# Performance work log

Hardware: AMD Instinct MI355X
Metric: run time of the kernel (lower is better)

The kernel has to match this reference:

```python
import jax, jax.numpy as jnp
import numpy as np

T = 2048
HID = 2048
H = 16
NOPE = 128
ROPE = 64
QKD = NOPE + ROPE  # 192
VD = 128
QLR = 1536
KVLR = 512
IDX_H = 32
IDX_D = 128
TOPK = 512
EPS = 1e-6
SCALING = QKD ** -0.5


def rms_norm(x, w):
    return x * jax.lax.rsqrt(jnp.mean(x * x, axis=-1, keepdims=True) + EPS) * w


def layer_norm(x, g, b):
    mu = jnp.mean(x, axis=-1, keepdims=True)
    var = jnp.mean((x - mu) ** 2, axis=-1, keepdims=True)
    return (x - mu) * jax.lax.rsqrt(var + EPS) * g + b


def apply_rope(x, positions, base=10000.0):
    # non-neox (interleaved) rotary; x: [..., d] with leading token axis
    d = x.shape[-1]
    inv = 1.0 / (base ** (jnp.arange(0, d, 2, dtype=jnp.float32) / d))
    f = positions.astype(jnp.float32)[:, None] * inv  # [T, d/2]
    shp = (x.shape[0],) + (1,) * (x.ndim - 2) + (d // 2,)
    cos, sin = jnp.cos(f).reshape(shp), jnp.sin(f).reshape(shp)
    x1, x2 = x[..., ::2], x[..., 1::2]
    return jnp.stack([x1 * cos - x2 * sin, x1 * sin + x2 * cos], axis=-1).reshape(x.shape)


def setup_inputs() -> dict:
    key = jax.random.key(0)
    ks = jax.random.split(key, 10)
    s = 0.02
    return {
        "positions": jnp.arange(T, dtype=jnp.int64) if jax.config.jax_enable_x64 else jnp.arange(T, dtype=jnp.int32),
        "hidden_states": jax.random.normal(ks[0], (T, HID), jnp.float32),
        "w_qkv_a": jax.random.normal(ks[1], (HID, QLR + KVLR + ROPE), jnp.float32) * s,
        "q_a_ln_w": jnp.ones((QLR,), jnp.float32),
        "w_qb": jax.random.normal(ks[2], (QLR, H * QKD), jnp.float32) * s,
        "kv_a_ln_w": jnp.ones((KVLR,), jnp.float32),
        "w_kvb": jax.random.normal(ks[3], (KVLR, H * (NOPE + VD)), jnp.float32) * s,
        "w_o": jax.random.normal(ks[4], (H * VD, HID), jnp.float32) * s,
        "w_idx_qb": jax.random.normal(ks[5], (QLR, IDX_H * IDX_D), jnp.float32) * s,
        "w_idx_k": jax.random.normal(ks[6], (HID, IDX_D), jnp.float32) * s,
        "idx_k_gamma": jnp.ones((IDX_D,), jnp.float32),
        "idx_k_beta": jnp.zeros((IDX_D,), jnp.float32),
        "w_wproj": jax.random.normal(ks[7], (HID, IDX_H), jnp.float32) * s,
        "b_wproj": jnp.zeros((IDX_H,), jnp.float32),
    }


def _forward(positions, hidden_states, w_qkv_a, q_a_ln_w, w_qb, kv_a_ln_w, w_kvb,
             w_o, w_idx_qb, w_idx_k, idx_k_gamma, idx_k_beta, w_wproj, b_wproj):
    t = hidden_states.shape[0]
    # fused low-rank projections
    qkv = hidden_states @ w_qkv_a
    q_c, kv_c, k_pe = jnp.split(qkv, [QLR, QLR + KVLR], axis=-1)
    q_c = rms_norm(q_c, q_a_ln_w)           # hidden_states_or_q_c
    kv_cn = rms_norm(kv_c, kv_a_ln_w)

    # ---- Indexer (lightning top-k token selection) ----
    qi = (q_c @ w_idx_qb).reshape(t, IDX_H, IDX_D)
    qi_pe, qi_nope = qi[..., :ROPE], qi[..., ROPE:]
    ki = layer_norm(hidden_states @ w_idx_k, idx_k_gamma, idx_k_beta)  # [T, IDX_D]
    ki_pe, ki_nope = ki[..., :ROPE], ki[..., ROPE:]
    qi = jnp.concatenate([apply_rope(qi_pe, positions), qi_nope], axis=-1)
    ki = jnp.concatenate([apply_rope(ki_pe, positions), ki_nope], axis=-1)
    w = (hidden_states @ w_wproj + b_wproj) * (IDX_D ** -0.5) * (IDX_H ** -0.5)  # [T, IDX_H]
    logits = jax.nn.relu(jnp.einsum('thd,sd->ths', qi, ki))   # [T, IDX_H, T]
    score = jnp.einsum('th,ths->ts', w, logits)               # [T, T]
    causal = jnp.tril(jnp.ones((t, t), bool))
    neg = jnp.finfo(score.dtype).min
    score = jnp.where(causal, score, neg)
    _, topk_idx = jax.lax.top_k(score, TOPK)                  # [T, TOPK]
    sel = jnp.zeros((t, t), bool).at[jnp.arange(t)[:, None], topk_idx].set(True)
    mask = causal & sel

    # ---- MLA attention ----
    q = (q_c @ w_qb).reshape(t, H, QKD)
    q_nope, q_pe = q[..., :NOPE], q[..., NOPE:]
    q_pe = apply_rope(q_pe, positions)
    k_pe_r = apply_rope(k_pe, positions)                      # [T, ROPE], shared across heads
    kv = (kv_cn @ w_kvb).reshape(t, H, NOPE + VD)
    k_nope, v = kv[..., :NOPE], kv[..., NOPE:]
    q_full = jnp.concatenate([q_nope, q_pe], axis=-1)         # [T, H, QKD]
    k_full = jnp.concatenate([k_nope, jnp.broadcast_to(k_pe_r[:, None, :], (t, H, ROPE))], axis=-1)
    attn = jnp.einsum('thd,shd->hts', q_full, k_full) * SCALING
    attn = jnp.where(mask[None], attn, neg)
    p = jax.nn.softmax(attn, axis=-1)
    out = jnp.einsum('hts,shv->thv', p, v).reshape(t, H * VD)
    return out @ w_o


def reference(positions, hidden_states, w_qkv_a, q_a_ln_w, w_qb, kv_a_ln_w, w_kvb,
              w_o, w_idx_qb, w_idx_k, idx_k_gamma, idx_k_beta, w_wproj, b_wproj):
    return _forward(positions, hidden_states, w_qkv_a, q_a_ln_w, w_qb, kv_a_ln_w,
                    w_kvb, w_o, w_idx_qb, w_idx_k, idx_k_gamma, idx_k_beta,
                    w_wproj, b_wproj)
```

## Files before the change

### kernel.cpp

```cpp
#include <hip/hip_runtime.h>
#include <cfloat>
#include <cmath>

#define T_    2048
#define HID_  2048
#define QKVN_ 2112
#define QKVX_ 2272
#define QLR_  1536
#define KVLR_ 512
#define ROPE_ 64
#define NOPE_ 128
#define QKD_  192
#define VD_   128
#define H_    16
#define IDXH_ 32
#define IDXD_ 128
#define TOPK_ 512
#define EPS_  1e-6f
#define SCALING_ 0.07216878364870323f

typedef unsigned int u32;
typedef unsigned short u16;
typedef __bf16 bf16x8 __attribute__((ext_vector_type(8)));
typedef _Float16 f16;
typedef f16 f16x8 __attribute__((ext_vector_type(8)));
typedef float f32x4 __attribute__((ext_vector_type(4)));

__device__ __forceinline__ u16 f2bf(float x) {
  u32 u = __float_as_uint(x);
  u32 r = (u + 0x7fffu + ((u >> 16) & 1u)) >> 16;
  return (u16)r;
}
__device__ __forceinline__ float bf2f(u16 h) { return __uint_as_float(((u32)h) << 16); }
__device__ __forceinline__ u32 pack2(float a, float b) { return (u32)f2bf(a) | ((u32)f2bf(b) << 16); }
__device__ __forceinline__ bf16x8 ld8(const void* p) { return *(const bf16x8*)p; }
__device__ __forceinline__ f32x4 mfma16(bf16x8 a, bf16x8 b, f32x4 c) {
  return __builtin_amdgcn_mfma_f32_16x16x32_bf16(a, b, c, 0, 0, 0);
}
__device__ __forceinline__ u16 hbits(f16 h) { union { f16 h; u16 u; } c; c.h = h; return c.u; }
__device__ __forceinline__ u32 hpack(f16 a, f16 b) { return (u32)hbits(a) | ((u32)hbits(b) << 16); }
__device__ __forceinline__ f16x8 ldh8(const void* p) { return *(const f16x8*)p; }
__device__ __forceinline__ f32x4 mfmah(f16x8 a, f16x8 b, f32x4 c) {
  return __builtin_amdgcn_mfma_f32_16x16x32_f16(a, b, c, 0, 0, 0);
}
__device__ __forceinline__ void gload16(const u16* g, u16* l) {
  __builtin_amdgcn_global_load_lds(
      (__attribute__((address_space(1))) void*)(g),
      (__attribute__((address_space(3))) void*)(l), 16, 0, 0);
}

__global__ __launch_bounds__(256) void rope_tab_kernel(float2* __restrict__ tab) {
  int i = blockIdx.x * 256 + threadIdx.x;
  if (i >= T_ * 32) return;
  int t = i >> 5, j = i & 31;
  float inv = powf(10000.f, -(float)j * (1.f / 32.f));
  float f = (float)t * inv;
  tab[i] = make_float2(cosf(f), sinf(f));
}
__device__ __forceinline__ void rope_apply(float2 cs, float& x0, float& x1) {
  float a = x0, b = x1;
  x0 = a * cs.x - b * cs.y;
  x1 = a * cs.y + b * cs.x;
}

struct TSJob { const float* src; u16* oh; u16* ol; int K; int N; };
__global__ __launch_bounds__(256) void transpose_split_multi(
    TSJob j0, TSJob j1, TSJob j2, TSJob j3) {
  TSJob jb = (blockIdx.z == 0) ? j0 : (blockIdx.z == 1) ? j1 : (blockIdx.z == 2) ? j2 : j3;
  int k0 = blockIdx.y * 64, n0 = blockIdx.x * 64;
  if (k0 >= jb.K || n0 >= jb.N) return;
  __shared__ float t[64][65];
  for (int j = 0; j < 16; ++j) {
    int u = threadIdx.x + 256 * j; int r = u >> 6, c = u & 63;
    t[r][c] = (k0 + r < jb.K && n0 + c < jb.N) ? jb.src[(size_t)(k0 + r) * jb.N + n0 + c] : 0.f;
  }
  __syncthreads();
  for (int j = 0; j < 16; ++j) {
    int u = threadIdx.x + 256 * j; int r = u >> 6, c = u & 63;
    if (n0 + r < jb.N && k0 + c < jb.K) {
      float v = t[c][r];
      f16 h = (f16)v;
      jb.oh[(size_t)(n0 + r) * jb.K + k0 + c] = hbits(h);
      jb.ol[(size_t)(n0 + r) * jb.K + k0 + c] = hbits((f16)(v - (float)h));
    }
  }
}

struct TBJob { const float* src; u16* out; int K; int N; };
__global__ __launch_bounds__(256) void transpose_bf16_multi(TBJob j0, TBJob j1, TBJob j2) {
  TBJob jb = (blockIdx.z == 0) ? j0 : (blockIdx.z == 1) ? j1 : j2;
  int k0 = blockIdx.y * 64, n0 = blockIdx.x * 64;
  if (k0 >= jb.K || n0 >= jb.N) return;
  __shared__ float t[64][65];
  for (int j = 0; j < 16; ++j) {
    int u = threadIdx.x + 256 * j; int r = u >> 6, c = u & 63;
    t[r][c] = (k0 + r < jb.K && n0 + c < jb.N) ? jb.src[(size_t)(k0 + r) * jb.N + n0 + c] : 0.f;
  }
  __syncthreads();
  for (int j = 0; j < 16; ++j) {
    int u = threadIdx.x + 256 * j; int r = u >> 6, c = u & 63;
    if (n0 + r < jb.N && k0 + c < jb.K) jb.out[(size_t)(n0 + r) * jb.K + k0 + c] = f2bf(t[c][r]);
  }
}

__global__ __launch_bounds__(256) void split_f16_k(
    const float* __restrict__ in, u16* __restrict__ hi, u16* __restrict__ lo, long n) {
  for (long i = ((long)blockIdx.x * 256 + threadIdx.x) * 4; i < n; i += (long)gridDim.x * 1024) {
    float4 v = *(const float4*)(in + i);
    f16 a = (f16)v.x, b = (f16)v.y, c = (f16)v.z, d = (f16)v.w;
    *(u32*)(hi + i) = hpack(a, b);
    *(u32*)(hi + i + 2) = hpack(c, d);
    *(u32*)(lo + i) = hpack((f16)(v.x - (float)a), (f16)(v.y - (float)b));
    *(u32*)(lo + i + 2) = hpack((f16)(v.z - (float)c), (f16)(v.w - (float)d));
  }
}

__global__ __launch_bounds__(256) void conv_bf16_k(
    const float* __restrict__ in, u16* __restrict__ out, long n) {
  for (long i = ((long)blockIdx.x * 256 + threadIdx.x) * 4; i < n; i += (long)gridDim.x * 1024) {
    float4 v = *(const float4*)(in + i);
    *(u32*)(out + i) = pack2(v.x, v.y);
    *(u32*)(out + i + 2) = pack2(v.z, v.w);
  }
}

__global__ __launch_bounds__(256) void gemm_hl(
    const u16* __restrict__ Ah_, const u16* __restrict__ Al_, int lda,
    const u16* __restrict__ Bh_, const u16* __restrict__ Bl_, int ldb,
    float* __restrict__ C, int ldc, const float* __restrict__ bias, int bcol0,
    float bscale, int N, int K) {
  __shared__ u32 Ah[128][16], Al[128][16], Bh[128][16], Bl[128][16];
  const int tid = threadIdx.x;
  const int bm = blockIdx.y * 128, bn = blockIdx.x * 128;
  const int wid = tid >> 6, lane = tid & 63, wr = wid >> 1, wc = wid & 1;
  const int lr = lane & 15, lg = lane >> 4;
  const u16* srcb = (wid == 0) ? Ah_ : (wid == 1) ? Al_ : (wid == 2) ? Bh_ : Bl_;
  const int sld = (wid < 2) ? lda : ldb;
  const int rb = (wid < 2) ? bm : bn;
  u16* dst = (u16*)((wid == 0) ? &Ah[0][0] : (wid == 1) ? &Al[0][0]
                                           : (wid == 2) ? &Bh[0][0] : &Bl[0][0]);
  const int rowl = lane >> 2;
  const int offl = (lane & 3) * 8;
  f32x4 acc[4][4] = {};
  for (int k0 = 0; k0 < K; k0 += 32) {
#pragma unroll
    for (int c = 0; c < 8; ++c) {
      int gr = rb + c * 16 + rowl;
      if (wid >= 2) gr = min(gr, N - 1);
      gload16(srcb + (size_t)gr * sld + k0 + offl, dst + c * 512);
    }
    __syncthreads();
    f16x8 ah[4], al[4], bh[4], bl[4];
#pragma unroll
    for (int i = 0; i < 4; ++i) {
      ah[i] = ldh8(&Ah[wr * 64 + i * 16 + lr][lg * 4]);
      al[i] = ldh8(&Al[wr * 64 + i * 16 + lr][lg * 4]);
      bh[i] = ldh8(&Bh[wc * 64 + i * 16 + lr][lg * 4]);
      bl[i] = ldh8(&Bl[wc * 64 + i * 16 + lr][lg * 4]);
    }
#pragma unroll
    for (int i = 0; i < 4; ++i)
#pragma unroll
      for (int jn = 0; jn < 4; ++jn) {
        acc[i][jn] = mfmah(ah[i], bh[jn], acc[i][jn]);
        acc[i][jn] = mfmah(ah[i], bl[jn], acc[i][jn]);
        acc[i][jn] = mfmah(al[i], bh[jn], acc[i][jn]);
      }
    __syncthreads();
  }
#pragma unroll
  for (int i = 0; i < 4; ++i)
#pragma unroll
    for (int jn = 0; jn < 4; ++jn)
#pragma unroll
      for (int j = 0; j < 4; ++j) {
        int row = bm + wr * 64 + i * 16 + lg * 4 + j;
        int col = bn + wc * 64 + jn * 16 + lr;
        if (col < N) {
          float v = acc[i][jn][j];
          if (col >= bcol0) v = (v + bias[col - bcol0]) * bscale;
          C[(size_t)row * ldc + col] = v;
        }
      }
}

template <int CBF16>
__global__ __launch_bounds__(256) void gemm_t(
    const u16* __restrict__ Ab, int lda, long aoz,
    const u16* __restrict__ Bt, int ldb, long boz,
    void* __restrict__ Cp, int ldc, long coz, int N, int K) {
  __shared__ u32 As[128][16], Bs[128][16];
  const int tid = threadIdx.x;
  const int z = blockIdx.z;
  const int bm = blockIdx.y * 128, bn = blockIdx.x * 128;
  const int wid = tid >> 6, lane = tid & 63, wr = wid >> 1, wc = wid & 1;
  const int lr = lane & 15, lg = lane >> 4;
  const u16* A = Ab + aoz * z;
  const u16* B = Bt + boz * z;
  const u16* srcb = (wid < 2) ? A : B;
  const int sld = (wid < 2) ? lda : ldb;
  const int rb = (wid < 2) ? bm : bn;
  u16* dst = (u16*)((wid < 2) ? &As[0][0] : &Bs[0][0]);
  const int ccb = (wid & 1) * 4;
  const int rowl = lane >> 2;
  const int offl = (lane & 3) * 8;
  f32x4 acc[4][4] = {};
  for (int k0 = 0; k0 < K; k0 += 32) {
#pragma unroll
    for (int c = 0; c < 4; ++c) {
      int cc = ccb + c;
      int gr = rb + cc * 16 + rowl;
      if (wid >= 2) gr = min(gr, N - 1);
      gload16(srcb + (size_t)gr * sld + k0 + offl, dst + cc * 512);
    }
    __syncthreads();
    bf16x8 af[4], bf[4];
#pragma unroll
    for (int i = 0; i < 4; ++i) {
      af[i] = ld8(&As[wr * 64 + i * 16 + lr][lg * 4]);
      bf[i] = ld8(&Bs[wc * 64 + i * 16 + lr][lg * 4]);
    }
#pragma unroll
    for (int i = 0; i < 4; ++i)
#pragma unroll
      for (int jn = 0; jn < 4; ++jn)
        acc[i][jn] = mfma16(af[i], bf[jn], acc[i][jn]);
    __syncthreads();
  }
#pragma unroll
  for (int i = 0; i < 4; ++i)
#pragma unroll
    for (int jn = 0; jn < 4; ++jn)
#pragma unroll
      for (int j = 0; j < 4; ++j) {
        int row = bm + wr * 64 + i * 16 + lg * 4 + j;
        int col = bn + wc * 64 + jn * 16 + lr;
        if (col < N) {
          if (CBF16) ((u16*)Cp)[coz * z + (size_t)row * ldc + col] = f2bf(acc[i][jn][j]);
          else ((float*)Cp)[coz * z + (size_t)row * ldc + col] = acc[i][jn][j];
        }
      }
}

__global__ __launch_bounds__(256) void rmsnorm_kernel(
    const float* __restrict__ qkvx, const float* __restrict__ qw,
    const float* __restrict__ kvw, u16* __restrict__ qcb,
    u16* __restrict__ qch, u16* __restrict__ qcl, u16* __restrict__ kv_cn) {
  const int t = blockIdx.x, tid = threadIdx.x;
  const float* row = qkvx + (size_t)t * QKVX_;
  __shared__ float red[256];
  float ss = 0.f;
  for (int i = tid; i < QLR_; i += 256) { float v = row[i]; ss += v * v; }
  red[tid] = ss; __syncthreads();
  for (int s = 128; s; s >>= 1) { if (tid < s) red[tid] += red[tid + s]; __syncthreads(); }
  float scl = 1.0f / sqrtf(red[0] / (float)QLR_ + EPS_);
  for (int i = tid; i < QLR_; i += 256) {
    float val = row[i] * scl * qw[i];
    qcb[(size_t)t * QLR_ + i] = f2bf(val);
    f16 h = (f16)val;
    qch[(size_t)t * QLR_ + i] = hbits(h);
    qcl[(size_t)t * QLR_ + i] = hbits((f16)(val - (float)h));
  }
  __syncthreads();
  ss = 0.f;
  for (int i = tid; i < KVLR_; i += 256) { float v = row[QLR_ + i]; ss += v * v; }
  red[tid] = ss; __syncthreads();
  for (int s = 128; s; s >>= 1) { if (tid < s) red[tid] += red[tid + s]; __syncthreads(); }
  scl = 1.0f / sqrtf(red[0] / (float)KVLR_ + EPS_);
  for (int i = tid; i < KVLR_; i += 256)
    kv_cn[(size_t)t * KVLR_ + i] = f2bf(row[QLR_ + i] * scl * kvw[i]);
}

__global__ __launch_bounds__(256) void rope_qi_split_kernel(
    const float* __restrict__ qi, const float2* __restrict__ tab,
    u16* __restrict__ qih, u16* __restrict__ qil) {
  const int t = blockIdx.x, tid = threadIdx.x;
  const float* src = qi + (size_t)t * (IDXH_ * IDXD_);
  u16* dh = qih + (size_t)t * (IDXH_ * IDXD_);
  u16* dl = qil + (size_t)t * (IDXH_ * IDXD_);
  for (int p = tid; p < IDXH_ * IDXD_ / 2; p += 256) {
    int d = p & 63;
    float x0 = src[2 * p], x1 = src[2 * p + 1];
    if (d < 32) rope_apply(tab[t * 32 + d], x0, x1);
    f16 h0 = (f16)x0, h1 = (f16)x1;
    *(u32*)(dh + 2 * p) = hpack(h0, h1);
    *(u32*)(dl + 2 * p) = hpack((f16)(x0 - (float)h0), (f16)(x1 - (float)h1));
  }
}

__global__ __launch_bounds__(256) void rope_q_bf_kernel(
    u16* __restrict__ qfb, const float2* __restrict__ tab) {
  const int t = blockIdx.x, tid = threadIdx.x;
  for (int idx = tid; idx < H_ * 32; idx += 256) {
    int hh = idx / 32, j = idx % 32;
    u16* p = qfb + (size_t)t * (H_ * QKD_) + hh * QKD_ + NOPE_ + 2 * j;
    float x0 = bf2f(p[0]), x1 = bf2f(p[1]);
    rope_apply(tab[t * 32 + j], x0, x1);
    p[0] = f2bf(x0); p[1] = f2bf(x1);
  }
}

__global__ __launch_bounds__(64) void rope_kpe_kernel(
    const float* __restrict__ qkvx, const float2* __restrict__ tab,
    u16* __restrict__ kper) {
  const int t = blockIdx.x, tid = threadIdx.x;
  if (tid >= 32) return;
  const float* p = qkvx + (size_t)t * QKVX_ + (QLR_ + KVLR_);
  float x0 = p[2 * tid], x1 = p[2 * tid + 1];
  rope_apply(tab[t * 32 + tid], x0, x1);
  kper[(size_t)t * ROPE_ + 2 * tid] = f2bf(x0);
  kper[(size_t)t * ROPE_ + 2 * tid + 1] = f2bf(x1);
}

__global__ __launch_bounds__(128) void ki_ln_rope_kernel(
    const float* __restrict__ qkvx, const float* __restrict__ gamma,
    const float* __restrict__ beta, const float2* __restrict__ tab,
    u16* __restrict__ kih, u16* __restrict__ kil) {
  const int t = blockIdx.x, tid = threadIdx.x;
  __shared__ float x[128];
  __shared__ float red[128];
  float v = qkvx[(size_t)t * QKVX_ + QKVN_ + tid];
  red[tid] = v; __syncthreads();
  for (int s = 64; s; s >>= 1) { if (tid < s) red[tid] += red[tid + s]; __syncthreads(); }
  float mu = red[0] / 128.f;
  __syncthreads();
  float d = v - mu;
  red[tid] = d * d; __syncthreads();
  for (int s = 64; s; s >>= 1) { if (tid < s) red[tid] += red[tid + s]; __syncthreads(); }
  float var = red[0] / 128.f;
  float y = d * (1.0f / sqrtf(var + EPS_)) * gamma[tid] + beta[tid];
  x[tid] = y; __syncthreads();
  if (tid < 32) {
    float x0 = x[2 * tid], x1 = x[2 * tid + 1];
    rope_apply(tab[t * 32 + tid], x0, x1);
    x[2 * tid] = x0; x[2 * tid + 1] = x1;
  }
  __syncthreads();
  float fv = x[tid];
  f16 h = (f16)fv;
  kih[(size_t)t * IDXD_ + tid] = hbits(h);
  kil[(size_t)t * IDXD_ + tid] = hbits((f16)(fv - (float)h));
}

__global__ __launch_bounds__(256) void score_mfma(
    const u16* __restrict__ qih, const u16* __restrict__ qil,
    const u16* __restrict__ kih, const u16* __restrict__ kil,
    const float* __restrict__ wgt, int ldw, float* __restrict__ score) {
  const int s0 = blockIdx.x * 64, t0 = blockIdx.y * 64;
  if (s0 > t0 + 63) return;
  __shared__ u32 Kh[64][68], Kl[64][68], Qh[64][68], Ql[64][68];
  __shared__ float wts[64][33];
  const int tid = threadIdx.x;
  const int wid = tid >> 6, lane = tid & 63, wr = wid >> 1, wc = wid & 1;
  const int lr = lane & 15, lg = lane >> 4;
#pragma unroll
  for (int j = 0; j < 4; ++j) {
    int u = tid + 256 * j; int row = u >> 4, p = u & 15;
    *(uint4*)&Kh[row][p * 4] = *(const uint4*)(kih + (size_t)(s0 + row) * IDXD_ + p * 8);
    *(uint4*)&Kl[row][p * 4] = *(const uint4*)(kil + (size_t)(s0 + row) * IDXD_ + p * 8);
  }
#pragma unroll
  for (int j = 0; j < 8; ++j) {
    int u = tid + 256 * j; int r = u >> 5, c = u & 31;
    wts[r][c] = wgt[(size_t)(t0 + r) * ldw + c];
  }
  __syncthreads();
  f16x8 bh[2][4], bl[2][4];
#pragma unroll
  for (int ni = 0; ni < 2; ++ni)
#pragma unroll
    for (int kb = 0; kb < 4; ++kb) {
      bh[ni][kb] = ldh8(&Kh[wc * 32 + ni * 16 + lr][kb * 16 + lg * 4]);
      bl[ni][kb] = ldh8(&Kl[wc * 32 + ni * 16 + lr][kb * 16 + lg * 4]);
    }
  f32x4 fin[2][2] = {};
  for (int h = 0; h < IDXH_; ++h) {
#pragma unroll
    for (int j = 0; j < 4; ++j) {
      int u = tid + 256 * j; int row = u >> 4, p = u & 15;
      size_t g = (size_t)(t0 + row) * (IDXH_ * IDXD_) + h * IDXD_ + p * 8;
      *(uint4*)&Qh[row][p * 4] = *(const uint4*)(qih + g);
      *(uint4*)&Ql[row][p * 4] = *(const uint4*)(qil + g);
    }
    __syncthreads();
    f32x4 acch[2][2] = {};
#pragma unroll
    for (int kb = 0; kb < 4; ++kb) {
      f16x8 ah0 = ldh8(&Qh[wr * 32 + lr][kb * 16 + lg * 4]);
      f16x8 ah1 = ldh8(&Qh[wr * 32 + 16 + lr][kb * 16 + lg * 4]);
      f16x8 al0 = ldh8(&Ql[wr * 32 + lr][kb * 16 + lg * 4]);
      f16x8 al1 = ldh8(&Ql[wr * 32 + 16 + lr][kb * 16 + lg * 4]);
#pragma unroll
      for (int ni = 0; ni < 2; ++ni) {
        acch[0][ni] = mfmah(ah0, bh[ni][kb], acch[0][ni]);
        acch[0][ni] = mfmah(ah0, bl[ni][kb], acch[0][ni]);
        acch[0][ni] = mfmah(al0, bh[ni][kb], acch[0][ni]);
        acch[1][ni] = mfmah(ah1, bh[ni][kb], acch[1][ni]);
        acch[1][ni] = mfmah(ah1, bl[ni][kb], acch[1][ni]);
        acch[1][ni] = mfmah(al1, bh[ni][kb], acch[1][ni]);
      }
    }
#pragma unroll
    for (int mi = 0; mi < 2; ++mi)
#pragma unroll
      for (int j = 0; j < 4; ++j) {
        float w = wts[wr * 32 + mi * 16 + lg * 4 + j][h];
        fin[mi][0][j] += w * fmaxf(acch[mi][0][j], 0.f);
        fin[mi][1][j] += w * fmaxf(acch[mi][1][j], 0.f);
      }
    __syncthreads();
  }
#pragma unroll
  for (int mi = 0; mi < 2; ++mi)
#pragma unroll
    for (int ni = 0; ni < 2; ++ni)
#pragma unroll
      for (int j = 0; j < 4; ++j) {
        int row = t0 + wr * 32 + mi * 16 + lg * 4 + j;
        int col = s0 + wc * 32 + ni * 16 + lr;
        score[(size_t)row * T_ + col] = fin[mi][ni][j];
      }
}

__global__ __launch_bounds__(256) void topk_kernel(
    const float* __restrict__ score, int* __restrict__ selidx,
    int* __restrict__ selcnt) {
  const int t = blockIdx.x;
  const int L = t + 1;
  const int tid = threadIdx.x;
  if (L <= TOPK_) {
    for (int j = tid; j < TOPK_; j += 256)
      selidx[(size_t)t * TOPK_ + j] = (j < L) ? j : 0;
    if (tid == 0) selcnt[t] = L;
    return;
  }
  __shared__ unsigned u[T_];
  __shared__ unsigned hist[16];
  __shared__ unsigned sprefix;
  __shared__ int sk;
  __shared__ int part[256];
  for (int i = tid; i < T_; i += 256) {
    float v = (i < L) ? score[(size_t)t * T_ + i] : -FLT_MAX;
    unsigned b = __float_as_uint(v);
    u[i] = (b & 0x80000000u) ? ~b : (b | 0x80000000u);
  }
  if (tid == 0) { sprefix = 0u; sk = TOPK_; }
  __syncthreads();
  for (int pass = 0; pass < 8; ++pass) {
    const int shift = 28 - 4 * pass;
    if (tid < 16) hist[tid] = 0u;
    __syncthreads();
    unsigned pfx = sprefix;
    for (int i = tid; i < L; i += 256) {
      unsigned val = u[i];
      bool match = (pass == 0) || ((val >> (shift + 4)) == pfx);
      if (match) atomicAdd(&hist[(val >> shift) & 15u], 1u);
    }
    __syncthreads();
    if (tid == 0) {
      int k = sk; unsigned cum = 0u; int bsel = 0;
      for (int bb = 15; bb >= 0; --bb) {
        if (cum + hist[bb] >= (unsigned)k) { bsel = bb; sk = k - (int)cum; break; }
        cum += hist[bb];
      }
      sprefix = (sprefix << 4) | (unsigned)bsel;
    }
    __syncthreads();
  }
  const unsigned thr = sprefix;
  const int kEq = sk;
  const int base = tid * 8;
  int eqloc[8]; int esum = 0;
  for (int r = 0; r < 8; ++r) {
    int i = base + r;
    int f = (i < L && u[i] == thr) ? 1 : 0;
    eqloc[r] = esum; esum += f;
  }
  part[tid] = esum; __syncthreads();
  for (int off = 1; off < 256; off <<= 1) {
    int v = (tid >= off) ? part[tid - off] : 0;
    __syncthreads();
    part[tid] += v;
    __syncthreads();
  }
  const int ebase = (tid > 0) ? part[tid - 1] : 0;
  __syncthreads();
  int sloc[8], selflag[8]; int ssum = 0;
  for (int r = 0; r < 8; ++r) {
    int i = base + r;
    int f = 0;
    if (i < L) {
      unsigned ui = u[i];
      if (ui > thr) f = 1;
      else if (ui == thr && (ebase + eqloc[r]) < kEq) f = 1;
    }
    selflag[r] = f; sloc[r] = ssum; ssum += f;
  }
  part[tid] = ssum; __syncthreads();
  for (int off = 1; off < 256; off <<= 1) {
    int v = (tid >= off) ? part[tid - off] : 0;
    __syncthreads();
    part[tid] += v;
    __syncthreads();
  }
  const int sbase = (tid > 0) ? part[tid - 1] : 0;
  for (int r = 0; r < 8; ++r)
    if (selflag[r]) selidx[(size_t)t * TOPK_ + sbase + sloc[r]] = base + r;
  if (tid == 0) selcnt[t] = TOPK_;
}

__global__ __launch_bounds__(256, 3) void attn_mla_kernel(
    const u16* __restrict__ qeff, const u16* __restrict__ qfb,
    const u16* __restrict__ kvcn, const u16* __restrict__ kper,
    const int* __restrict__ selidx, const int* __restrict__ selcnt,
    u16* __restrict__ Olat) {
  const int t = blockIdx.x;
  const int tid = threadIdx.x;
  const int wid = tid >> 6, lane = tid & 63;
  const int lr = lane & 15, lg = lane >> 4;
  __shared__ int sidxs[512];
  __shared__ u16 Pb[16][520];
  __shared__ u16 SB[4][4096];
  __shared__ float redm[4][16];
  __shared__ float reds[4][16];
  const int cnt = selcnt[t];
  for (int j = tid; j < 512; j += 256) sidxs[j] = selidx[(size_t)t * TOPK_ + j];
  __syncthreads();

  const int kl = lane >> 2;
  const int pcs = (((lane & 3) ^ ((lane >> 3) & 3))) << 3;
  const int rsw = ((lr >> 1) & 3) << 3;
  int skey[8];
#pragma unroll
  for (int j = 0; j < 8; ++j) skey[j] = sidxs[wid * 128 + j * 16 + kl];
  u16* ksw = &SB[wid][0];

  const u16* qe = qeff + (size_t)t * (H_ * 512) + lr * 512 + lg * 8;
  const u16* qp = qfb + (size_t)t * (H_ * QKD_) + lr * QKD_ + NOPE_ + lg * 8;
  bf16x8 qf[18];
#pragma unroll
  for (int kb = 0; kb < 16; ++kb) qf[kb] = ld8(qe + kb * 32);
  qf[16] = ld8(qp);
  qf[17] = ld8(qp + 32);

  f32x4 lgv[8] = {};
#pragma unroll
  for (int kb = 0; kb < 18; ++kb) {
    if (kb < 16) {
#pragma unroll
      for (int j = 0; j < 8; ++j)
        gload16(kvcn + (size_t)skey[j] * 512 + kb * 32 + pcs, ksw + j * 512);
    } else {
#pragma unroll
      for (int j = 0; j < 8; ++j)
        gload16(kper + (size_t)skey[j] * 64 + (kb - 16) * 32 + pcs, ksw + j * 512);
    }
    asm volatile("s_waitcnt vmcnt(0)" ::: "memory");
    __builtin_amdgcn_sched_barrier(0);
#pragma unroll
    for (int m = 0; m < 8; ++m) {
      bf16x8 kf = ld8(ksw + (m * 16 + lr) * 32 + (lg * 8 ^ rsw));
      lgv[m] = mfma16(kf, qf[kb], lgv[m]);
    }
    asm volatile("s_waitcnt lgkmcnt(0)" ::: "memory");
    __builtin_amdgcn_sched_barrier(0);
  }

  float mx = -FLT_MAX;
#pragma unroll
  for (int m = 0; m < 8; ++m)
#pragma unroll
    for (int j = 0; j < 4; ++j) {
      int slot = wid * 128 + m * 16 + lg * 4 + j;
      float v = (slot < cnt) ? lgv[m][j] * SCALING_ : -FLT_MAX;
      lgv[m][j] = v;
      mx = fmaxf(mx, v);
    }
  mx = fmaxf(mx, __shfl_xor(mx, 16));
  mx = fmaxf(mx, __shfl_xor(mx, 32));
  if (lane < 16) redm[wid][lane] = mx;
  __syncthreads();
  float hm = fmaxf(fmaxf(redm[0][lr], redm[1][lr]), fmaxf(redm[2][lr], redm[3][lr]));
  float sm = 0.f;
#pragma unroll
  for (int m = 0; m < 8; ++m)
#pragma unroll
    for (int j = 0; j < 4; ++j) {
      int slot = wid * 128 + m * 16 + lg * 4 + j;
      float e = (slot < cnt) ? expf(lgv[m][j] - hm) : 0.f;
      lgv[m][j] = e; sm += e;
    }
  sm += __shfl_xor(sm, 16);
  sm += __shfl_xor(sm, 32);
  if (lane < 16) reds[wid][lane] = sm;
  __syncthreads();
  float inv = 1.f / (reds[0][lr] + reds[1][lr] + reds[2][lr] + reds[3][lr]);
#pragma unroll
  for (int m = 0; m < 8; ++m) {
    int sl = wid * 128 + m * 16 + lg * 4;
    *(u32*)&Pb[lr][sl] = pack2(lgv[m][0] * inv, lgv[m][1] * inv);
    *(u32*)&Pb[lr][sl + 2] = pack2(lgv[m][2] * inv, lgv[m][3] * inv);
  }
  __syncthreads();

  u32* vpw = (u32*)&SB[wid][0];
  const int pl = lane >> 4;
  const int gq = lane & 15;
  const u16* vsrc = kvcn + wid * 128 + gq * 8;
  f32x4 oacc[8] = {};
  uint4 ra[4], rb[4];
#pragma unroll
  for (int s = 0; s < 4; ++s) {
    int p = s * 4 + pl;
    ra[s] = *(const uint4*)(vsrc + (size_t)sidxs[2 * p] * 512);
    rb[s] = *(const uint4*)(vsrc + (size_t)sidxs[2 * p + 1] * 512);
  }
  for (int c = 0; c < 16; ++c) {
#pragma unroll
    for (int s = 0; s < 4; ++s) {
      int p = s * 4 + pl;
      int col = (gq * 8) ^ ((s & 3) << 3);
      const u16* A = (const u16*)&ra[s];
      const u16* B = (const u16*)&rb[s];
      u32 w[8];
#pragma unroll
      for (int j = 0; j < 8; ++j) w[j] = (u32)A[j] | ((u32)B[j] << 16);
      *(uint4*)&vpw[p * 128 + col] = make_uint4(w[0], w[1], w[2], w[3]);
      *(uint4*)&vpw[p * 128 + col + 4] = make_uint4(w[4], w[5], w[6], w[7]);
    }
    if (c < 15) {
#pragma unroll
      for (int s = 0; s < 4; ++s) {
        int p = s * 4 + pl;
        ra[s] = *(const uint4*)(vsrc + (size_t)sidxs[(c + 1) * 32 + 2 * p] * 512);
        rb[s] = *(const uint4*)(vsrc + (size_t)sidxs[(c + 1) * 32 + 2 * p + 1] * 512);
      }
    }
    bf16x8 pa = ld8(&Pb[lr][c * 32 + lg * 8]);
    union BB { u32 u[4]; bf16x8 v; };
    BB bb[8];
#pragma unroll
    for (int C = 0; C < 8; ++C) {
      int col = (C * 16 + lr) ^ (lg << 3);
#pragma unroll
      for (int e = 0; e < 4; ++e)
        bb[C].u[e] = vpw[(lg * 4 + e) * 128 + col];
    }
    __builtin_amdgcn_s_setprio(1);
#pragma unroll
    for (int C = 0; C < 8; ++C) oacc[C] = mfma16(pa, bb[C].v, oacc[C]);
    __builtin_amdgcn_s_setprio(0);
  }
#pragma unroll
  for (int C = 0; C < 8; ++C)
#pragma unroll
    for (int j = 0; j < 4; ++j) {
      int h = lg * 4 + j;
      Olat[(size_t)t * (H_ * 512) + h * 512 + wid * 128 + C * 16 + lr] = f2bf(oacc[C][j]);
    }
}

extern "C" void kernel_launch(void* const* d_in, const int* in_sizes, int n_in,
                              void* d_out, int out_size, void* d_ws, size_t ws_size,
                              hipStream_t stream) {
  const float* hidden    = (const float*)d_in[1];
  const float* w_qkv_a   = (const float*)d_in[2];
  const float* q_a_ln_w  = (const float*)d_in[3];
  const float* w_qb      = (const float*)d_in[4];
  const float* kv_a_ln_w = (const float*)d_in[5];
  const float* w_kvb     = (const float*)d_in[6];
  const float* w_o       = (const float*)d_in[7];
  const float* w_idx_qb  = (const float*)d_in[8];
  const float* w_idx_k   = (const float*)d_in[9];
  const float* idx_g     = (const float*)d_in[10];
  const float* idx_b     = (const float*)d_in[11];
  const float* w_wproj   = (const float*)d_in[12];
  const float* b_wproj   = (const float*)d_in[13];

  char* W = (char*)d_ws;
  size_t o = 0;
  auto alloc = [&](size_t bytes) { void* p = W + o; o += (bytes + 255) & ~(size_t)255; return p; };
  u16* qcb     = (u16*)alloc((size_t)T_ * QLR_ * 2);
  u16* kv_cn   = (u16*)alloc((size_t)T_ * KVLR_ * 2);
  u16* kper    = (u16*)alloc((size_t)T_ * ROPE_ * 2);
  int* selidx  = (int*)alloc((size_t)T_ * TOPK_ * 4);
  int* selcnt  = (int*)alloc((size_t)T_ * 4);
  u16* kih     = (u16*)alloc((size_t)T_ * IDXD_ * 2);
  u16* kil     = (u16*)alloc((size_t)T_ * IDXD_ * 2);
  u16* hidh    = (u16*)alloc((size_t)T_ * HID_ * 2);
  u16* hidl    = (u16*)alloc((size_t)T_ * HID_ * 2);
  float2* rtab = (float2*)alloc((size_t)T_ * 32 * 8);
  u16* qch     = (u16*)alloc((size_t)T_ * QLR_ * 2);
  u16* qcl     = (u16*)alloc((size_t)T_ * QLR_ * 2);
  u16* wiqh    = (u16*)alloc((size_t)(IDXH_ * IDXD_) * QLR_ * 2);
  u16* wiql    = (u16*)alloc((size_t)(IDXH_ * IDXD_) * QLR_ * 2);
  u16* qih     = qch;
  u16* qil     = qch + (size_t)T_ * IDXH_ * IDXD_;
  float* qi    = (float*)alloc((size_t)T_ * IDXH_ * IDXD_ * 4);
  u16* qeff    = (u16*)qi;
  float* score = (float*)alloc((size_t)T_ * T_ * 4);
  u16* qfb     = (u16*)score;
  u16* attno   = (u16*)score;
  u16* wcath   = (u16*)alloc((size_t)QKVX_ * HID_ * 2);
  u16* wcatl   = (u16*)alloc((size_t)QKVX_ * HID_ * 2);
  float* qkvx  = (float*)alloc((size_t)T_ * QKVX_ * 4);
  u16* Olat    = wcath;
  u16* wqbt    = (u16*)alloc((size_t)(H_ * QKD_) * QLR_ * 2);
  u16* wkvb    = (u16*)alloc((size_t)KVLR_ * (H_ * 256) * 2);
  u16* wkvbt   = (u16*)alloc((size_t)(H_ * 256) * KVLR_ * 2);
  u16* wot     = (u16*)alloc((size_t)(H_ * VD_) * HID_ * 2);

  dim3 blk(256);
  auto g2 = [](int M, int N, int Z) { return dim3((N + 127) / 128, M / 128, Z); };

  rope_tab_kernel<<<(T_ * 32 + 255) / 256, blk, 0, stream>>>(rtab);
  {
    TSJob j0{w_qkv_a, wcath, wcatl, HID_, QKVN_};
    TSJob j1{w_idx_qb, wiqh, wiql, QLR_, IDXH_ * IDXD_};
    TSJob j2{w_idx_k, wcath + (size_t)QKVN_ * HID_, wcatl + (size_t)QKVN_ * HID_, HID_, IDXD_};
    TSJob j3{w_wproj, wcath + (size_t)(QKVN_ + IDXD_) * HID_, wcatl + (size_t)(QKVN_ + IDXD_) * HID_, HID_, IDXH_};
    transpose_split_multi<<<dim3(64, 32, 4), blk, 0, stream>>>(j0, j1, j2, j3);
  }
  {
    TBJob j0{w_qb, wqbt, QLR_, H_ * QKD_};
    TBJob j1{w_kvb, wkvbt, KVLR_, H_ * 256};
    TBJob j2{w_o, wot, H_ * VD_, HID_};
    transpose_bf16_multi<<<dim3(64, 32, 3), blk, 0, stream>>>(j0, j1, j2);
  }
  split_f16_k<<<2048, blk, 0, stream>>>(hidden, hidh, hidl, (long)T_ * HID_);
  conv_bf16_k<<<2048, blk, 0, stream>>>(w_kvb, wkvb, (long)KVLR_ * H_ * 256);

  gemm_hl<<<g2(T_, QKVX_, 1), blk, 0, stream>>>(
      hidh, hidl, HID_, wcath, wcatl, HID_, qkvx, QKVX_,
      b_wproj, QKVN_ + IDXD_, 0.015625f, QKVX_, HID_);
  rmsnorm_kernel<<<T_, blk, 0, stream>>>(qkvx, q_a_ln_w, kv_a_ln_w, qcb, qch, qcl, kv_cn);
  rope_kpe_kernel<<<T_, 64, 0, stream>>>(qkvx, rtab, kper);
  ki_ln_rope_kernel<<<T_, 128, 0, stream>>>(qkvx, idx_g, idx_b, rtab, kih, kil);

  gemm_hl<<<g2(T_, IDXH_ * IDXD_, 1), blk, 0, stream>>>(
      qch, qcl, QLR_, wiqh, wiql, QLR_, qi, IDXH_ * IDXD_,
      nullptr, 1 << 30, 1.f, IDXH_ * IDXD_, QLR_);
  rope_qi_split_kernel<<<T_, blk, 0, stream>>>(qi, rtab, qih, qil);

  score_mfma<<<dim3(32, 32), blk, 0, stream>>>(qih, qil, kih, kil,
                                               qkvx + QKVN_ + IDXD_, QKVX_, score);
  topk_kernel<<<T_, blk, 0, stream>>>(score, selidx, selcnt);

  gemm_t<1><<<g2(T_, H_ * QKD_, 1), blk, 0, stream>>>(qcb, QLR_, 0, wqbt, QLR_, 0, qfb, H_ * QKD_, 0, H_ * QKD_, QLR_);
  rope_q_bf_kernel<<<T_, blk, 0, stream>>>(qfb, rtab);
  gemm_t<1><<<g2(T_, 512, H_), blk, 0, stream>>>(qfb, H_ * QKD_, QKD_, wkvb, H_ * 256, 256, qeff, H_ * 512, 512, 512, NOPE_);
  attn_mla_kernel<<<T_, blk, 0, stream>>>(qeff, qfb, kv_cn, kper, selidx, selcnt, Olat);
  gemm_t<1><<<g2(T_, VD_, H_), blk, 0, stream>>>(Olat, H_ * 512, 512, wkvbt + 128 * 512, KVLR_, 256 * 512, attno, H_ * VD_, VD_, VD_, 512);
  gemm_t<0><<<g2(T_, HID_, 1), blk, 0, stream>>>(attno, H_ * VD_, 0, wot, H_ * VD_, 0, d_out, HID_, 0, HID_, H_ * VD_);
}
```

Before: 667.6 us.

## Double-buffer gathered K loads in MLA attention logits and pad V staging rows

The logits loop now splits each wave's K staging area into two half-buffers and processes 36 half-steps. It issues the gathered global loads for step s+2 while step s computes, waiting only on the older batch with vmcnt(4) instead of draining all loads each iteration. This hides gather latency behind MFMA work. It also pads the V packing stride from 128 to 132 words, which is meant to cut LDS bank conflicts. The padding grows shared memory per block and could affect the 3-blocks-per-CU occupancy target.

```diff
diff --git a/kernel.cpp b/kernel.cpp
--- a/kernel.cpp
+++ b/kernel.cpp
@@ -520,7 +520,7 @@
   const int lr = lane & 15, lg = lane >> 4;
   __shared__ int sidxs[512];
   __shared__ u16 Pb[16][520];
-  __shared__ u16 SB[4][4096];
+  __shared__ __align__(16) u16 SB[4][4224];
   __shared__ float redm[4][16];
   __shared__ float reds[4][16];
   const int cnt = selcnt[t];
@@ -533,7 +533,8 @@
   int skey[8];
 #pragma unroll
   for (int j = 0; j < 8; ++j) skey[j] = sidxs[wid * 128 + j * 16 + kl];
-  u16* ksw = &SB[wid][0];
+  u16* buf0 = &SB[wid][0];
+  u16* buf1 = &SB[wid][2048];
 
   const u16* qe = qeff + (size_t)t * (H_ * 512) + lr * 512 + lg * 8;
   const u16* qp = qfb + (size_t)t * (H_ * QKD_) + lr * QKD_ + NOPE_ + lg * 8;
@@ -545,25 +546,39 @@
 
   f32x4 lgv[8] = {};
 #pragma unroll
-  for (int kb = 0; kb < 18; ++kb) {
-    if (kb < 16) {
-#pragma unroll
-      for (int j = 0; j < 8; ++j)
-        gload16(kvcn + (size_t)skey[j] * 512 + kb * 32 + pcs, ksw + j * 512);
-    } else {
-#pragma unroll
-      for (int j = 0; j < 8; ++j)
-        gload16(kper + (size_t)skey[j] * 64 + (kb - 16) * 32 + pcs, ksw + j * 512);
-    }
-    asm volatile("s_waitcnt vmcnt(0)" ::: "memory");
+  for (int j = 0; j < 4; ++j)
+    gload16(kvcn + (size_t)skey[j] * 512 + pcs, buf0 + j * 512);
+#pragma unroll
+  for (int j = 0; j < 4; ++j)
+    gload16(kvcn + (size_t)skey[4 + j] * 512 + pcs, buf1 + j * 512);
+#pragma unroll
+  for (int s = 0; s < 36; ++s) {
+    const int kb = s >> 1, h = s & 1;
+    u16* b = (h == 0) ? buf0 : buf1;
+    if (s == 35) { asm volatile("s_waitcnt vmcnt(0)" ::: "memory"); }
+    else         { asm volatile("s_waitcnt vmcnt(4)" ::: "memory"); }
     __builtin_amdgcn_sched_barrier(0);
-#pragma unroll
-    for (int m = 0; m < 8; ++m) {
-      bf16x8 kf = ld8(ksw + (m * 16 + lr) * 32 + (lg * 8 ^ rsw));
-      lgv[m] = mfma16(kf, qf[kb], lgv[m]);
-    }
+    bf16x8 kf[4];
+#pragma unroll
+    for (int i = 0; i < 4; ++i)
+      kf[i] = ld8(b + (i * 16 + lr) * 32 + (lg * 8 ^ rsw));
+#pragma unroll
+    for (int i = 0; i < 4; ++i)
+      lgv[h * 4 + i] = mfma16(kf[i], qf[kb], lgv[h * 4 + i]);
     asm volatile("s_waitcnt lgkmcnt(0)" ::: "memory");
     __builtin_amdgcn_sched_barrier(0);
+    if (s + 2 < 36) {
+      const int kb2 = (s + 2) >> 1;
+      if (kb2 < 16) {
+#pragma unroll
+        for (int j = 0; j < 4; ++j)
+          gload16(kvcn + (size_t)skey[h * 4 + j] * 512 + kb2 * 32 + pcs, b + j * 512);
+      } else {
+#pragma unroll
+        for (int j = 0; j < 4; ++j)
+          gload16(kper + (size_t)skey[h * 4 + j] * 64 + (kb2 - 16) * 32 + pcs, b + j * 512);
+      }
+    }
   }
 
   float mx = -FLT_MAX;
@@ -625,8 +640,8 @@
       u32 w[8];
 #pragma unroll
       for (int j = 0; j < 8; ++j) w[j] = (u32)A[j] | ((u32)B[j] << 16);
-      *(uint4*)&vpw[p * 128 + col] = make_uint4(w[0], w[1], w[2], w[3]);
-      *(uint4*)&vpw[p * 128 + col + 4] = make_uint4(w[4], w[5], w[6], w[7]);
+      *(uint4*)&vpw[p * 132 + col] = make_uint4(w[0], w[1], w[2], w[3]);
+      *(uint4*)&vpw[p * 132 + col + 4] = make_uint4(w[4], w[5], w[6], w[7]);
     }
     if (c < 15) {
 #pragma unroll
@@ -644,7 +659,7 @@
       int col = (C * 16 + lr) ^ (lg << 3);
 #pragma unroll
       for (int e = 0; e < 4; ++e)
-        bb[C].u[e] = vpw[(lg * 4 + e) * 128 + col];
+        bb[C].u[e] = vpw[(lg * 4 + e) * 132 + col];
     }
     __builtin_amdgcn_s_setprio(1);
 #pragma unroll
```

Result: no change. 663.0 us (median of 2 runs) (-0.7%).
